# Kernel tuning notes

Hardware: AMD Instinct MI355X
Metric: run time of the kernel (lower is better)

Reference implementation:

```python
import jax, jax.numpy as jnp
import numpy as np

B, D, L, O = 131072, 128, 4, 1  # batch, d_model, num_layers(depths), estimator out dim


def setup_inputs() -> dict:
    key = jax.random.key(0)
    k0, k1, k2, k3 = jax.random.split(key, 4)
    x = jax.random.normal(k0, (B, D), jnp.float32)
    Wr = jax.random.normal(k1, (D, L), jnp.float32) * (1.0 / np.sqrt(D))
    W_layers = jax.random.normal(k2, (L, 2 * D, D), jnp.float32) * (1.0 / np.sqrt(2 * D))
    b_layers = jnp.zeros((L, D), jnp.float32)
    W_est = jax.random.normal(k3, (L, D, O), jnp.float32) * (1.0 / np.sqrt(D))
    b_est = jnp.zeros((L, O), jnp.float32)
    return {"x": x, "Wr": Wr, "W_layers": W_layers, "b_layers": b_layers,
            "W_est": W_est, "b_est": b_est}


def reference(x, Wr, W_layers, b_layers, W_est, b_est):
    # Router on stop_gradient(inputs); ReLU gate -> genuinely sparse gates (>0 test).
    gates = jax.nn.relu(jax.lax.stop_gradient(x) @ Wr)  # [B, L]

    def compute(last_out, depth):
        # layer depth: Dense on [last_layer_output, init_input]
        cur = jax.nn.relu(
            jnp.concatenate([last_out, x], axis=-1) @ W_layers[depth] + b_layers[depth]
        )  # [B, D]
        preds = cur @ W_est[depth] + b_est[depth]  # estimator at this depth, [B, O]
        if depth == L - 1:
            return preds
        # SparseDispatcher2D over 2 experts (exit / enter). combine() is an
        # unsorted_segment_sum over tokens with gate > 0 (unweighted), which is
        # exactly a 0/1-mask sum per token -- dense, jit-friendly equivalent.
        mask_exit = (gates[:, depth] > 0.0).astype(cur.dtype)[:, None]
        mask_enter = (jnp.sum(gates[:, depth + 1:], axis=1) > 0.0).astype(cur.dtype)[:, None]
        return mask_exit * preds + mask_enter * compute(cur, depth + 1)

    return compute(x, 0)
```

## Files before the change

### kernel.cpp

```cpp
#include <hip/hip_runtime.h>
#include <cstddef>

typedef float f4 __attribute__((ext_vector_type(4)));
typedef __bf16 bf16x8 __attribute__((ext_vector_type(8)));
typedef __bf16 bf16x4 __attribute__((ext_vector_type(4)));
typedef float f32x16 __attribute__((ext_vector_type(16)));

constexpr int D_ = 128;
constexpr int LAYERS = 4;
constexpr int BM = 128;
constexpr int NT = 512;
constexpr int ROWB = 512;

__device__ __forceinline__ int swz(int row, int woff) {
    return row * ROWB + (woff ^ ((row & 15) << 4));
}

__global__ void prep(const float* __restrict__ Wl, __bf16* __restrict__ wt2) {
    int idx = blockIdx.x * 256 + threadIdx.x;
    int j = idx & 7, lane = (idx >> 3) & 63, kc = (idx >> 9) & 15,
        nf = (idx >> 13) & 3, d = idx >> 15;
    int n  = nf * 32 + (lane & 31);
    int ks = kc * 16 + (lane >> 5) * 8 + j;
    float v;
    if (d == 0)
        v = (ks < 128) ? 0.f
                       : (Wl[(size_t)(ks - 128) * D_ + n] + Wl[(size_t)ks * D_ + n]);
    else
        v = Wl[(size_t)d * 2 * D_ * D_ + (size_t)ks * D_ + n];
    wt2[idx] = (__bf16)v;
}

__global__ __launch_bounds__(NT, 4)
void moe_fwd(const float* __restrict__ x, const float* __restrict__ Wr,
             const __bf16* __restrict__ wt2, const float* __restrict__ bl,
             const float* __restrict__ We, const float* __restrict__ be,
             float* __restrict__ out)
{
    __shared__ char Ab[BM * ROWB];
    __shared__ float PR[4][BM];
    __shared__ float CSM[BM][4];

    const int t    = threadIdx.x;
    const int m0   = blockIdx.x * BM;
    const int lane = t & 63, w = t >> 6;
    const int nf   = w >> 1;
    const int tw   = w & 1;
    const int lo5  = lane & 31, hi = lane >> 5;
    const int hi16 = hi * 16;
    const int tok0 = tw * 64 + lo5, tok1 = tok0 + 32;
    const int grp  = t >> 4, il = t & 15;

    f4 wrv[8];
    #pragma unroll
    for (int j = 0; j < 8; ++j)
        wrv[j] = *(const f4*)(Wr + (il * 8 + j) * 4);

    #pragma unroll
    for (int i = 0; i < 4; ++i) {
        const int row = i * 32 + grp;
        const f4* gx = (const f4*)(x + (size_t)(m0 + row) * D_ + il * 8);
        f4 lo = gx[0], hp = gx[1];
        bf16x8 v;
        v[0] = (__bf16)lo[0]; v[1] = (__bf16)lo[1]; v[2] = (__bf16)lo[2]; v[3] = (__bf16)lo[3];
        v[4] = (__bf16)hp[0]; v[5] = (__bf16)hp[1]; v[6] = (__bf16)hp[2]; v[7] = (__bf16)hp[3];
        *(bf16x8*)(Ab + swz(row, 256 + il * 16)) = v;

        double a0 = 0, a1 = 0, a2 = 0, a3 = 0;
        #pragma unroll
        for (int j = 0; j < 4; ++j) {
            double xv = (double)lo[j];
            a0 += xv * (double)wrv[j][0]; a1 += xv * (double)wrv[j][1];
            a2 += xv * (double)wrv[j][2]; a3 += xv * (double)wrv[j][3];
        }
        #pragma unroll
        for (int j = 0; j < 4; ++j) {
            double xv = (double)hp[j];
            a0 += xv * (double)wrv[4 + j][0]; a1 += xv * (double)wrv[4 + j][1];
            a2 += xv * (double)wrv[4 + j][2]; a3 += xv * (double)wrv[4 + j][3];
        }
        #pragma unroll
        for (int s = 1; s < 16; s <<= 1) {
            a0 += __shfl_xor(a0, s, 16);
            a1 += __shfl_xor(a1, s, 16);
            a2 += __shfl_xor(a2, s, 16);
            a3 += __shfl_xor(a3, s, 16);
        }
        if (il == 0) {
            f4 c;
            c[0] = a0 > 0.0 ? 1.f : 0.f; c[1] = a1 > 0.0 ? 1.f : 0.f;
            c[2] = a2 > 0.0 ? 1.f : 0.f; c[3] = a3 > 0.0 ? 1.f : 0.f;
            *(f4*)(&CSM[row][0]) = c;
        }
    }

    float outc = 0.f;
    __syncthreads();

    #pragma unroll
    for (int d = 0; d < LAYERS; ++d) {
        const int kstart = (d == 0) ? 8 : 0;

        bf16x8 wf[16];
        {
            const __bf16* wb = wt2 + ((size_t)(d * 4 + nf) * 16) * 512 + lane * 8;
            #pragma unroll
            for (int kc = 0; kc < 16; ++kc)
                if (kc >= kstart)
                    wf[kc] = *(const bf16x8*)(wb + (size_t)kc * 512);
        }

        f32x16 acc[2];
        #pragma unroll
        for (int tf = 0; tf < 2; ++tf)
            #pragma unroll
            for (int j = 0; j < 16; ++j) acc[tf][j] = 0.f;

        #pragma unroll
        for (int ks = 0; ks < 16; ++ks) {
            if (ks < kstart) continue;
            int wo = ks * 32 + hi16;
            bf16x8 b0 = *(const bf16x8*)(Ab + swz(tok0, wo));
            bf16x8 b1 = *(const bf16x8*)(Ab + swz(tok1, wo));
            acc[0] = __builtin_amdgcn_mfma_f32_32x32x16_bf16(wf[ks], b0, acc[0], 0, 0, 0);
            acc[1] = __builtin_amdgcn_mfma_f32_32x32x16_bf16(wf[ks], b1, acc[1], 0, 0, 0);
        }
        __syncthreads();

        float p0 = 0.f, p1 = 0.f;
        #pragma unroll
        for (int rg = 0; rg < 4; ++rg) {
            int nb = nf * 32 + rg * 8 + hi * 4;
            f4 bv = *(const f4*)(bl + d * D_ + nb);
            f4 ev = *(const f4*)(We + d * D_ + nb);
            #pragma unroll
            for (int tf = 0; tf < 2; ++tf) {
                float c0 = fmaxf(acc[tf][rg * 4 + 0] + bv[0], 0.f);
                float c1 = fmaxf(acc[tf][rg * 4 + 1] + bv[1], 0.f);
                float c2 = fmaxf(acc[tf][rg * 4 + 2] + bv[2], 0.f);
                float c3 = fmaxf(acc[tf][rg * 4 + 3] + bv[3], 0.f);
                float pp = c0 * ev[0] + c1 * ev[1] + c2 * ev[2] + c3 * ev[3];
                if (tf == 0) p0 += pp; else p1 += pp;
                if (d < LAYERS - 1) {
                    bf16x4 cc;
                    cc[0] = (__bf16)c0; cc[1] = (__bf16)c1;
                    cc[2] = (__bf16)c2; cc[3] = (__bf16)c3;
                    int token = tw * 64 + tf * 32 + lo5;
                    *(bf16x4*)(Ab + swz(token, nb * 2)) = cc;
                }
            }
        }
        p0 += __shfl_xor(p0, 32, 64);
        p1 += __shfl_xor(p1, 32, 64);
        if (lane < 32) {
            PR[nf][tw * 64 + lo5]      = p0;
            PR[nf][tw * 64 + 32 + lo5] = p1;
        }
        __syncthreads();

        if (t < BM)
            outc += CSM[t][d] * (PR[0][t] + PR[1][t] + PR[2][t] + PR[3][t] + be[d]);
    }

    if (t < BM) out[m0 + t] = outc;
}

extern "C" void kernel_launch(void* const* d_in, const int* in_sizes, int n_in,
                              void* d_out, int out_size, void* d_ws, size_t ws_size,
                              hipStream_t stream) {
    const float* x  = (const float*)d_in[0];
    const float* Wr = (const float*)d_in[1];
    const float* Wl = (const float*)d_in[2];
    const float* bl = (const float*)d_in[3];
    const float* We = (const float*)d_in[4];
    const float* be = (const float*)d_in[5];
    float* out = (float*)d_out;
    __bf16* wt2 = (__bf16*)d_ws;
    const int B = in_sizes[0] / D_;

    prep<<<dim3(512), dim3(256), 0, stream>>>(Wl, wt2);
    moe_fwd<<<dim3(B / BM), dim3(NT), 0, stream>>>(x, Wr, wt2, bl, We, be, out);
}
```

Measured before the change: 54.27 us.

## Halve block tile to 64 rows and stream weight fragments per k-step

The block tile shrinks from 128 to 64 tokens, so each wave now issues one MFMA per k-step instead of two. The 16-entry weight-fragment register array and the Wr router registers are replaced by loads issued inside the k loop. This cuts register and LDS pressure so that launch bounds can request 8 blocks per CU, trading the per-wave reuse of each weight fragment across two token tiles for higher occupancy. Weight traffic from L2 doubles relative to the amount of compute.

```diff
diff --git a/kernel.cpp b/kernel.cpp
--- a/kernel.cpp
+++ b/kernel.cpp
@@ -8,7 +8,7 @@
 
 constexpr int D_ = 128;
 constexpr int LAYERS = 4;
-constexpr int BM = 128;
+constexpr int BM = 64;
 constexpr int NT = 512;
 constexpr int ROWB = 512;
 
@@ -31,7 +31,7 @@
     wt2[idx] = (__bf16)v;
 }
 
-__global__ __launch_bounds__(NT, 4)
+__global__ __launch_bounds__(NT, 8)
 void moe_fwd(const float* __restrict__ x, const float* __restrict__ Wr,
              const __bf16* __restrict__ wt2, const float* __restrict__ bl,
              const float* __restrict__ We, const float* __restrict__ be,
@@ -48,16 +48,11 @@
     const int tw   = w & 1;
     const int lo5  = lane & 31, hi = lane >> 5;
     const int hi16 = hi * 16;
-    const int tok0 = tw * 64 + lo5, tok1 = tok0 + 32;
+    const int tok0 = tw * 32 + lo5;
     const int grp  = t >> 4, il = t & 15;
 
-    f4 wrv[8];
     #pragma unroll
-    for (int j = 0; j < 8; ++j)
-        wrv[j] = *(const f4*)(Wr + (il * 8 + j) * 4);
-
-    #pragma unroll
-    for (int i = 0; i < 4; ++i) {
+    for (int i = 0; i < 2; ++i) {
         const int row = i * 32 + grp;
         const f4* gx = (const f4*)(x + (size_t)(m0 + row) * D_ + il * 8);
         f4 lo = gx[0], hp = gx[1];
@@ -69,15 +64,17 @@
         double a0 = 0, a1 = 0, a2 = 0, a3 = 0;
         #pragma unroll
         for (int j = 0; j < 4; ++j) {
+            f4 wv = *(const f4*)(Wr + (il * 8 + j) * 4);
             double xv = (double)lo[j];
-            a0 += xv * (double)wrv[j][0]; a1 += xv * (double)wrv[j][1];
-            a2 += xv * (double)wrv[j][2]; a3 += xv * (double)wrv[j][3];
+            a0 += xv * (double)wv[0]; a1 += xv * (double)wv[1];
+            a2 += xv * (double)wv[2]; a3 += xv * (double)wv[3];
         }
         #pragma unroll
         for (int j = 0; j < 4; ++j) {
+            f4 wv = *(const f4*)(Wr + (il * 8 + 4 + j) * 4);
             double xv = (double)hp[j];
-            a0 += xv * (double)wrv[4 + j][0]; a1 += xv * (double)wrv[4 + j][1];
-            a2 += xv * (double)wrv[4 + j][2]; a3 += xv * (double)wrv[4 + j][3];
+            a0 += xv * (double)wv[0]; a1 += xv * (double)wv[1];
+            a2 += xv * (double)wv[2]; a3 += xv * (double)wv[3];
         }
         #pragma unroll
         for (int s = 1; s < 16; s <<= 1) {
@@ -99,63 +96,40 @@
 
     #pragma unroll
     for (int d = 0; d < LAYERS; ++d) {
-        const int kstart = (d == 0) ? 8 : 0;
+        f32x16 acc;
+        #pragma unroll
+        for (int j = 0; j < 16; ++j) acc[j] = 0.f;
 
-        bf16x8 wf[16];
-        {
-            const __bf16* wb = wt2 + ((size_t)(d * 4 + nf) * 16) * 512 + lane * 8;
-            #pragma unroll
-            for (int kc = 0; kc < 16; ++kc)
-                if (kc >= kstart)
-                    wf[kc] = *(const bf16x8*)(wb + (size_t)kc * 512);
-        }
-
-        f32x16 acc[2];
-        #pragma unroll
-        for (int tf = 0; tf < 2; ++tf)
-            #pragma unroll
-            for (int j = 0; j < 16; ++j) acc[tf][j] = 0.f;
-
+        const __bf16* wb = wt2 + ((size_t)(d * 4 + nf) * 16) * 512 + lane * 8;
         #pragma unroll
         for (int ks = 0; ks < 16; ++ks) {
-            if (ks < kstart) continue;
-            int wo = ks * 32 + hi16;
-            bf16x8 b0 = *(const bf16x8*)(Ab + swz(tok0, wo));
-            bf16x8 b1 = *(const bf16x8*)(Ab + swz(tok1, wo));
-            acc[0] = __builtin_amdgcn_mfma_f32_32x32x16_bf16(wf[ks], b0, acc[0], 0, 0, 0);
-            acc[1] = __builtin_amdgcn_mfma_f32_32x32x16_bf16(wf[ks], b1, acc[1], 0, 0, 0);
+            if (ks < (d == 0 ? 8 : 0)) continue;
+            bf16x8 wf = *(const bf16x8*)(wb + (size_t)ks * 512);
+            bf16x8 b0 = *(const bf16x8*)(Ab + swz(tok0, ks * 32 + hi16));
+            acc = __builtin_amdgcn_mfma_f32_32x32x16_bf16(wf, b0, acc, 0, 0, 0);
         }
         __syncthreads();
 
-        float p0 = 0.f, p1 = 0.f;
+        float p = 0.f;
         #pragma unroll
         for (int rg = 0; rg < 4; ++rg) {
             int nb = nf * 32 + rg * 8 + hi * 4;
             f4 bv = *(const f4*)(bl + d * D_ + nb);
             f4 ev = *(const f4*)(We + d * D_ + nb);
-            #pragma unroll
-            for (int tf = 0; tf < 2; ++tf) {
-                float c0 = fmaxf(acc[tf][rg * 4 + 0] + bv[0], 0.f);
-                float c1 = fmaxf(acc[tf][rg * 4 + 1] + bv[1], 0.f);
-                float c2 = fmaxf(acc[tf][rg * 4 + 2] + bv[2], 0.f);
-                float c3 = fmaxf(acc[tf][rg * 4 + 3] + bv[3], 0.f);
-                float pp = c0 * ev[0] + c1 * ev[1] + c2 * ev[2] + c3 * ev[3];
-                if (tf == 0) p0 += pp; else p1 += pp;
-                if (d < LAYERS - 1) {
-                    bf16x4 cc;
-                    cc[0] = (__bf16)c0; cc[1] = (__bf16)c1;
-                    cc[2] = (__bf16)c2; cc[3] = (__bf16)c3;
-                    int token = tw * 64 + tf * 32 + lo5;
-                    *(bf16x4*)(Ab + swz(token, nb * 2)) = cc;
-                }
+            float c0 = fmaxf(acc[rg * 4 + 0] + bv[0], 0.f);
+            float c1 = fmaxf(acc[rg * 4 + 1] + bv[1], 0.f);
+            float c2 = fmaxf(acc[rg * 4 + 2] + bv[2], 0.f);
+            float c3 = fmaxf(acc[rg * 4 + 3] + bv[3], 0.f);
+            p += c0 * ev[0] + c1 * ev[1] + c2 * ev[2] + c3 * ev[3];
+            if (d < LAYERS - 1) {
+                bf16x4 cc;
+                cc[0] = (__bf16)c0; cc[1] = (__bf16)c1;
+                cc[2] = (__bf16)c2; cc[3] = (__bf16)c3;
+                *(bf16x4*)(Ab + swz(tok0, nb * 2)) = cc;
             }
         }
-        p0 += __shfl_xor(p0, 32, 64);
-        p1 += __shfl_xor(p1, 32, 64);
-        if (lane < 32) {
-            PR[nf][tw * 64 + lo5]      = p0;
-            PR[nf][tw * 64 + 32 + lo5] = p1;
-        }
+        p += __shfl_xor(p, 32, 64);
+        if (lane < 32) PR[nf][tok0] = p;
         __syncthreads();
 
         if (t < BM)
```

After: 87.96 us. 62.1% more time.

## Software-pipeline weight fragment loads with an 8-deep register ring and explicit vmcnt waits

Applied to the files above, without the earlier changes.

Replaces the per-layer load of all 16 weight fragments with an 8-register ring fed by inline-asm global loads and explicit s_waitcnt vmcnt counts. The next layer's first half is prefetched right after the MFMA loop, so those loads overlap the epilogue and barriers. It also cuts live VGPRs from 16 fragments to 8 and hoists the b_est loads. The risk is that inline asm hides the loads from the compiler's waitcnt tracking, so correctness depends on hand-counted outstanding loads. Other global loads such as bl/We in the epilogue would also disturb those counts.

```diff
diff --git a/kernel.cpp b/kernel.cpp
--- a/kernel.cpp
+++ b/kernel.cpp
@@ -31,6 +31,32 @@
     wt2[idx] = (__bf16)v;
 }
 
+#define MFMA32(A, B, C) __builtin_amdgcn_mfma_f32_32x32x16_bf16((A), (B), (C), 0, 0, 0)
+
+__device__ __forceinline__ void gload(bf16x8& dst, const __bf16* p) {
+    asm volatile("global_load_dwordx4 %0, %1, off" : "=v"(dst) : "v"(p));
+}
+template<int N>
+__device__ __forceinline__ void vwait(bf16x8& x) {
+    if constexpr (N >= 7)      asm volatile("s_waitcnt vmcnt(7)" : "+v"(x));
+    else if constexpr (N == 6) asm volatile("s_waitcnt vmcnt(6)" : "+v"(x));
+    else if constexpr (N == 5) asm volatile("s_waitcnt vmcnt(5)" : "+v"(x));
+    else if constexpr (N == 4) asm volatile("s_waitcnt vmcnt(4)" : "+v"(x));
+    else if constexpr (N == 3) asm volatile("s_waitcnt vmcnt(3)" : "+v"(x));
+    else if constexpr (N == 2) asm volatile("s_waitcnt vmcnt(2)" : "+v"(x));
+    else if constexpr (N == 1) asm volatile("s_waitcnt vmcnt(1)" : "+v"(x));
+    else                       asm volatile("s_waitcnt vmcnt(0)" : "+v"(x));
+}
+
+#define KSTEP(WQ, ks, NW) do {                                           \
+    vwait<NW>(WQ);                                                       \
+    bf16x8 b0_ = *(const bf16x8*)(Ab + swz(tok0, (ks) * 32 + hi16));     \
+    bf16x8 b1_ = *(const bf16x8*)(Ab + swz(tok1, (ks) * 32 + hi16));     \
+    acc0 = MFMA32(WQ, b0_, acc0);                                        \
+    acc1 = MFMA32(WQ, b1_, acc1);                                        \
+    if ((ks) + 8 < 16) gload(WQ, wb + (size_t)((ks) + 8) * 512);         \
+} while (0)
+
 __global__ __launch_bounds__(NT, 4)
 void moe_fwd(const float* __restrict__ x, const float* __restrict__ Wr,
              const __bf16* __restrict__ wt2, const float* __restrict__ bl,
@@ -95,37 +121,48 @@
     }
 
     float outc = 0.f;
+    const f4 bev = *(const f4*)be;
     __syncthreads();
+
+    const __bf16* wb = wt2 + ((size_t)(0 * 4 + nf) * 16) * 512 + lane * 8;
+    bf16x8 wqa, wqb, wqc, wqd, wqe, wqf, wqg, wqh;
+    gload(wqa, wb + (size_t) 8 * 512);
+    gload(wqb, wb + (size_t) 9 * 512);
+    gload(wqc, wb + (size_t)10 * 512);
+    gload(wqd, wb + (size_t)11 * 512);
+    gload(wqe, wb + (size_t)12 * 512);
+    gload(wqf, wb + (size_t)13 * 512);
+    gload(wqg, wb + (size_t)14 * 512);
+    gload(wqh, wb + (size_t)15 * 512);
 
     #pragma unroll
     for (int d = 0; d < LAYERS; ++d) {
-        const int kstart = (d == 0) ? 8 : 0;
-
-        bf16x8 wf[16];
-        {
-            const __bf16* wb = wt2 + ((size_t)(d * 4 + nf) * 16) * 512 + lane * 8;
-            #pragma unroll
-            for (int kc = 0; kc < 16; ++kc)
-                if (kc >= kstart)
-                    wf[kc] = *(const bf16x8*)(wb + (size_t)kc * 512);
-        }
-
-        f32x16 acc[2];
-        #pragma unroll
-        for (int tf = 0; tf < 2; ++tf)
-            #pragma unroll
-            for (int j = 0; j < 16; ++j) acc[tf][j] = 0.f;
-
-        #pragma unroll
-        for (int ks = 0; ks < 16; ++ks) {
-            if (ks < kstart) continue;
-            int wo = ks * 32 + hi16;
-            bf16x8 b0 = *(const bf16x8*)(Ab + swz(tok0, wo));
-            bf16x8 b1 = *(const bf16x8*)(Ab + swz(tok1, wo));
-            acc[0] = __builtin_amdgcn_mfma_f32_32x32x16_bf16(wf[ks], b0, acc[0], 0, 0, 0);
-            acc[1] = __builtin_amdgcn_mfma_f32_32x32x16_bf16(wf[ks], b1, acc[1], 0, 0, 0);
+        f32x16 acc0, acc1;
+        #pragma unroll
+        for (int j = 0; j < 16; ++j) { acc0[j] = 0.f; acc1[j] = 0.f; }
+
+        if (d == 0) {
+            KSTEP(wqa,  8, 7); KSTEP(wqb,  9, 6); KSTEP(wqc, 10, 5); KSTEP(wqd, 11, 4);
+            KSTEP(wqe, 12, 3); KSTEP(wqf, 13, 2); KSTEP(wqg, 14, 1); KSTEP(wqh, 15, 0);
+        } else {
+            KSTEP(wqa,  0, 7); KSTEP(wqb,  1, 7); KSTEP(wqc,  2, 7); KSTEP(wqd,  3, 7);
+            KSTEP(wqe,  4, 7); KSTEP(wqf,  5, 7); KSTEP(wqg,  6, 7); KSTEP(wqh,  7, 7);
+            KSTEP(wqa,  8, 7); KSTEP(wqb,  9, 6); KSTEP(wqc, 10, 5); KSTEP(wqd, 11, 4);
+            KSTEP(wqe, 12, 3); KSTEP(wqf, 13, 2); KSTEP(wqg, 14, 1); KSTEP(wqh, 15, 0);
         }
         __syncthreads();
+
+        if (d < LAYERS - 1) {
+            wb = wt2 + ((size_t)((d + 1) * 4 + nf) * 16) * 512 + lane * 8;
+            gload(wqa, wb + (size_t)0 * 512);
+            gload(wqb, wb + (size_t)1 * 512);
+            gload(wqc, wb + (size_t)2 * 512);
+            gload(wqd, wb + (size_t)3 * 512);
+            gload(wqe, wb + (size_t)4 * 512);
+            gload(wqf, wb + (size_t)5 * 512);
+            gload(wqg, wb + (size_t)6 * 512);
+            gload(wqh, wb + (size_t)7 * 512);
+        }
 
         float p0 = 0.f, p1 = 0.f;
         #pragma unroll
@@ -135,10 +172,11 @@
             f4 ev = *(const f4*)(We + d * D_ + nb);
             #pragma unroll
             for (int tf = 0; tf < 2; ++tf) {
-                float c0 = fmaxf(acc[tf][rg * 4 + 0] + bv[0], 0.f);
-                float c1 = fmaxf(acc[tf][rg * 4 + 1] + bv[1], 0.f);
-                float c2 = fmaxf(acc[tf][rg * 4 + 2] + bv[2], 0.f);
-                float c3 = fmaxf(acc[tf][rg * 4 + 3] + bv[3], 0.f);
+                const f32x16& at = tf ? acc1 : acc0;
+                float c0 = fmaxf(at[rg * 4 + 0] + bv[0], 0.f);
+                float c1 = fmaxf(at[rg * 4 + 1] + bv[1], 0.f);
+                float c2 = fmaxf(at[rg * 4 + 2] + bv[2], 0.f);
+                float c3 = fmaxf(at[rg * 4 + 3] + bv[3], 0.f);
                 float pp = c0 * ev[0] + c1 * ev[1] + c2 * ev[2] + c3 * ev[3];
                 if (tf == 0) p0 += pp; else p1 += pp;
                 if (d < LAYERS - 1) {
@@ -159,7 +197,7 @@
         __syncthreads();
 
         if (t < BM)
-            outc += CSM[t][d] * (PR[0][t] + PR[1][t] + PR[2][t] + PR[3][t] + be[d]);
+            outc += CSM[t][d] * (PR[0][t] + PR[1][t] + PR[2][t] + PR[3][t] + bev[d]);
     }
 
     if (t < BM) out[m0 + t] = outc;
```

Result: slower. 56.90 us (+4.8%).
